# Kernel tuning notes

Hardware: AMD Instinct MI355X
Metric: run time of the kernel (lower is better)

## Reference

```python
import jax, jax.numpy as jnp
import numpy as np

NUM_HEADS = 12
SS_ATTN_ITER = 1
EPS = 1e-12  # F.normalize default eps


def _l2norm(x):
    n = jnp.linalg.norm(x, axis=-1, keepdims=True)
    return x / jnp.maximum(n, EPS)


def setup_inputs() -> dict:
    key = jax.random.key(0)
    k1, k2, k3, k4 = jax.random.split(key, 4)
    N, B, C = 1569, 8, 768
    x = jax.random.normal(k1, (N, B, C), dtype=jnp.float32)
    Wqkv = jax.random.normal(k2, (3 * C, C), dtype=jnp.float32) * 0.02
    Wproj = jax.random.normal(k3, (C, C), dtype=jnp.float32) * 0.02
    bproj = jax.random.normal(k4, (C,), dtype=jnp.float32) * 0.02
    return {"x": x, "Wqkv": Wqkv, "Wproj": Wproj, "bproj": bproj}


def _forward(x, Wqkv, Wproj, bproj):
    # x: [N, B, C] -> [B, N, C] (module does x.transpose(0, 1))
    xb = jnp.swapaxes(x, 0, 1)
    B, N, C = xb.shape
    H = NUM_HEADS
    hd = C // H
    scale = hd ** (-0.5)

    # qkv projection (no bias), split into per-head q, k, v: [B, H, N, hd]
    qkv = (xb @ Wqkv.T).reshape(B, N, 3, H, hd)
    qkv = jnp.transpose(qkv, (2, 0, 3, 1, 4))
    q, k, v = qkv[0], qkv[1], qkv[2]

    # ---- original attention branch ----
    attn_ori = jax.nn.softmax(jnp.einsum('bhnd,bhmd->bhnm', q, k) * scale, axis=-1)
    x_ori = jnp.einsum('bhnm,bhmd->bhnd', attn_ori, v)
    x_ori = jnp.transpose(x_ori, (0, 2, 1, 3)).reshape(B, N, C)
    x_ori = x_ori @ Wproj.T + bproj

    # ---- self-self attention branches ----
    # inv_temp = mean over tokens of ||x||_2, per batch: [B, 1, 1, 1]
    pre_norm = jnp.mean(jnp.linalg.norm(xb, axis=-1), axis=-1)
    inv_temp = pre_norm[:, None, None, None] * scale

    def branch(xs):
        for _ in range(SS_ATTN_ITER):
            xs = _l2norm(xs)
            a = jax.nn.softmax(jnp.einsum('bhnd,bhmd->bhnm', xs, xs) * inv_temp, axis=-1)
            xs = jnp.einsum('bhnm,bhmd->bhnd', a, xs)
        xs = _l2norm(xs)
        a = jax.nn.softmax(jnp.einsum('bhnd,bhmd->bhnm', xs, xs) * inv_temp, axis=-1)
        return jnp.einsum('bhnm,bhmd->bhnd', a, v)

    xs = (branch(v) + branch(k) + branch(q)) / 3.0
    x_out = jnp.transpose(xs, (0, 2, 1, 3)).reshape(B, N, C)
    x_out = x_out @ Wproj.T + bproj

    # return in original [N, B, C] layout
    return jnp.swapaxes(x_out, 0, 1), jnp.swapaxes(x_ori, 0, 1)


def reference(x, Wqkv, Wproj, bproj):
    return _forward(x, Wqkv, Wproj, bproj)
```

## Files before the change

kernel.cpp:

```cpp
#include <hip/hip_runtime.h>
#include <stdint.h>

#define NTOK 1569
#define BB 8
#define CC 768
#define HH 12
#define HD 64
#define NBH (BB*HH)
#define NROW (NTOK*BB)
#define NCHUNK 25
#define NVEC (NBH*NTOK)
#define LASTV 33

typedef unsigned short ushort_t;
static const size_t SZ = (size_t)NROW * CC;

using f32x4 = __attribute__((ext_vector_type(4))) float;
using i32x4 = __attribute__((ext_vector_type(4))) int;
using i32x2 = __attribute__((ext_vector_type(2))) int;
using hfrag = __attribute__((ext_vector_type(8))) _Float16;

__device__ __forceinline__ float exp2_fast(float x){
  float r;
  asm("v_exp_f32 %0, %1" : "=v"(r) : "v"(x));
  return r;
}

__global__ __launch_bounds__(256) void prenorm_kernel(const float* __restrict__ x,
                                                      float* __restrict__ pre)
{
  const int b = blockIdx.y;
  const int wave = threadIdx.x >> 6, lane = threadIdx.x & 63;
  const int g = blockIdx.x * 4 + wave;
  float local = 0.f;
  for (int n = g; n < NTOK; n += 200){
    const float* xp = x + ((size_t)n * BB + b) * CC + lane * 4;
    float ss = 0.f;
    #pragma unroll
    for (int e = 0; e < 3; e++){
      f32x4 vv = *(const f32x4*)(xp + 256*e);
      ss += vv[0]*vv[0] + vv[1]*vv[1] + vv[2]*vv[2] + vv[3]*vv[3];
    }
    #pragma unroll
    for (int off = 1; off < 64; off <<= 1) ss += __shfl_xor(ss, off);
    local += sqrtf(ss);
  }
  if (lane == 0) atomicAdd(&pre[b], local);
}

__global__ __launch_bounds__(256) void cvt_f16(const float* __restrict__ in,
                                               ushort_t* __restrict__ out,
                                               int n8, float scl)
{
  const int i = blockIdx.x * 256 + threadIdx.x;
  if (i >= n8) return;
  const float* p = in + (size_t)i * 8;
  f32x4 a = *(const f32x4*)p, b = *(const f32x4*)(p + 4);
  union { _Float16 h[8]; i32x4 v; } u;
  #pragma unroll
  for (int e = 0; e < 4; e++){
    u.h[e]   = (_Float16)(a[e] * scl);
    u.h[4+e] = (_Float16)(b[e] * scl);
  }
  *(i32x4*)(out + (size_t)i * 8) = u.v;
}

__global__ __launch_bounds__(256) void gemm768(
    const ushort_t* __restrict__ A, const ushort_t* __restrict__ Bm,
    ushort_t* __restrict__ q, ushort_t* __restrict__ k, ushort_t* __restrict__ v,
    float* __restrict__ outp, const float* __restrict__ bias, int mode)
{
  __shared__ __align__(16) ushort_t As[8192];
  __shared__ __align__(16) ushort_t Bs[8192];

  const int mt = blockIdx.x, jt = blockIdx.y;
  const int tid = threadIdx.x;
  const int w = tid >> 6, lane = tid & 63;
  const int l16 = lane & 15, lq = lane >> 4;

  const int srow = tid & 127, shalf = tid >> 7;
  int ga = mt*128 + srow; if (ga > NROW-1) ga = NROW-1;
  const ushort_t* ap = A  + (size_t)ga * CC + shalf*32;
  const ushort_t* bp = Bm + (size_t)(jt*128 + srow) * CC + shalf*32;
  const int rb = srow >> 4, r16 = srow & 15;

  const int wr = (w >> 1) * 4, wc = (w & 1) * 4;

  f32x4 acc[4][4] = {};
  for (int kt = 0; kt < 12; kt++){
    #pragma unroll
    for (int i = 0; i < 4; i++){
      const int kq = shalf*4 + i;
      *(i32x4*)&As[((rb*8 + kq)*16 + r16)*8] = *(const i32x4*)(ap + kt*64 + i*8);
      *(i32x4*)&Bs[((rb*8 + kq)*16 + r16)*8] = *(const i32x4*)(bp + kt*64 + i*8);
    }
    __syncthreads();
    #pragma unroll
    for (int ks = 0; ks < 2; ks++){
      hfrag af[4], bf[4];
      #pragma unroll
      for (int rt = 0; rt < 4; rt++)
        af[rt] = *(const hfrag*)&As[(((wr+rt)*8 + ks*4 + lq)*16 + l16)*8];
      #pragma unroll
      for (int ct = 0; ct < 4; ct++)
        bf[ct] = *(const hfrag*)&Bs[(((wc+ct)*8 + ks*4 + lq)*16 + l16)*8];
      #pragma unroll
      for (int rt = 0; rt < 4; rt++)
        #pragma unroll
        for (int ct = 0; ct < 4; ct++)
          acc[rt][ct] = __builtin_amdgcn_mfma_f32_16x16x32_f16(af[rt], bf[ct], acc[rt][ct], 0, 0, 0);
    }
    __syncthreads();
  }

  const int mbase = mt*128 + (w >> 1)*64;
  const int jbase = jt*128 + (w & 1)*64;
  #pragma unroll
  for (int ct = 0; ct < 4; ct++){
    const int j = jbase + ct*16 + l16;
    if (mode == 0){
      const int s = j / 768, jj = j - s*768;
      const int h = jj >> 6, d = jj & 63;
      ushort_t* op = (s == 0) ? q : (s == 1) ? k : v;
      #pragma unroll
      for (int rt = 0; rt < 4; rt++)
        #pragma unroll
        for (int r = 0; r < 4; r++){
          const int m = mbase + rt*16 + lq*4 + r;
          if (m < NROW){
            const int n = m >> 3, b = m & 7;
            union { _Float16 h16; ushort_t u; } cv;
            cv.h16 = (_Float16)acc[rt][ct][r];
            op[((size_t)(b*HH + h) * NTOK + n) * HD + d] = cv.u;
          }
        }
    } else {
      const float bv = bias[j];
      #pragma unroll
      for (int rt = 0; rt < 4; rt++)
        #pragma unroll
        for (int r = 0; r < 4; r++){
          const int m = mbase + rt*16 + lq*4 + r;
          if (m < NROW) outp[(size_t)m * CC + j] = acc[rt][ct][r] + bv;
        }
    }
  }
}

__global__ __launch_bounds__(256) void l2norm_kernel(const ushort_t* __restrict__ in,
                                                     ushort_t* __restrict__ out,
                                                     int mode)
{
  const int vec = blockIdx.x * 8 + (threadIdx.x >> 5);
  const int lane = threadIdx.x & 31;
  if (vec >= NVEC) return;
  size_t iaddr;
  if (mode == 0){
    iaddr = (size_t)vec * HD + lane*2;
  } else {
    const int b = vec / (HH*NTOK);
    const int rem = vec - b*(HH*NTOK);
    const int h = rem / NTOK, n = rem - h*NTOK;
    iaddr = (size_t)(n*BB + b) * CC + h*HD + lane*2;
  }
  union { ushort_t u[2]; uint32_t pk; _Float16 h[2]; } uv;
  uv.pk = *(const uint32_t*)(in + iaddr);
  const float a = (float)uv.h[0], c = (float)uv.h[1];
  float ss = a*a + c*c;
  #pragma unroll
  for (int off = 1; off < 32; off <<= 1) ss += __shfl_xor(ss, off);
  const float inv = 1.0f / fmaxf(sqrtf(ss), 1e-12f);
  union { _Float16 h[2]; uint32_t pk; } ov;
  ov.h[0] = (_Float16)(a * inv);
  ov.h[1] = (_Float16)(c * inv);
  *(uint32_t*)(out + (size_t)vec * HD + lane*2) = ov.pk;
}

__global__ __launch_bounds__(256) void attn_mfma(
    const ushort_t* __restrict__ X, const ushort_t* __restrict__ Y,
    const ushort_t* __restrict__ Z, void* __restrict__ outp,
    const float* __restrict__ pre, float tf, int mode, int accum)
{
  __shared__ __align__(16) ushort_t Ks[64*64];
  __shared__ __align__(16) ushort_t Vt[64*64];
  __shared__ __align__(16) ushort_t Pt[128*64];

  const int lin  = blockIdx.y * 13 + blockIdx.x;
  const int nl   = (lin & 7) * 156 + (lin >> 3);
  const int bh   = nl / 13;
  const int qblk = nl - bh * 13;

  const int b = bh / HH, h = bh - (bh / HH) * HH;
  const float temp = (pre ? pre[b] * tf : tf) * 1.4426950408889634f;
  const size_t base = (size_t)bh * NTOK * HD;
  const int row0 = qblk * 128;
  const int tid = threadIdx.x;
  const int w = tid >> 6, lane = tid & 63;
  const int l16 = lane & 15, lq = lane >> 4;
  const int xk = (l16 & 7) << 4;

  hfrag qf[2][2];
  #pragma unroll
  for (int qt = 0; qt < 2; qt++){
    int r = row0 + w*32 + qt*16 + l16; if (r > NTOK-1) r = NTOK-1;
    const ushort_t* qp = X + base + (size_t)r*HD + lq*8;
    qf[qt][0] = *(const hfrag*)qp;
    qf[qt][1] = *(const hfrag*)(qp + 32);
  }

  const int skey = tid & 63, sseg = tid >> 6;
  const int kx = (skey & 7) << 4;
  const int vd2 = (tid & 31) * 2;
  const int vko = (tid >> 5) * 8;

  f32x4 acc[2][4] = {};
  float lsum[2] = {0.f, 0.f};

  for (int ch = 0; ch < NCHUNK; ch++){
    {
      int kg = ch*64 + skey; if (kg > NTOK-1) kg = NTOK-1;
      const ushort_t* kp = Y + base + (size_t)kg*HD + sseg*16;
      i32x4 kr0 = *(const i32x4*)kp;
      i32x4 kr1 = *(const i32x4*)(kp + 8);
      char* kbp = (char*)Ks + skey*128;
      *(i32x4*)(kbp + ((sseg*32     ) ^ kx)) = kr0;
      *(i32x4*)(kbp + ((sseg*32 + 16) ^ kx)) = kr1;

      uint32_t L[8];
      #pragma unroll
      for (int j = 0; j < 8; j++){
        int vg = ch*64 + vko + j; if (vg > NTOK-1) vg = NTOK-1;
        L[j] = *(const uint32_t*)(Z + base + (size_t)vg*HD + vd2);
      }
      i32x4 vlo, vhi;
      #pragma unroll
      for (int c = 0; c < 4; c++){
        const uint32_t A = L[2*c], B = L[2*c+1];
        vlo[c] = (int)((A & 0xffffu) | (B << 16));
        vhi[c] = (int)((A >> 16) | (B & 0xffff0000u));
      }
      char* vbp = (char*)Vt;
      *(i32x4*)(vbp + vd2*128     + ((vko*2) ^ ((vd2 & 7) << 4)))       = vlo;
      *(i32x4*)(vbp + (vd2+1)*128 + ((vko*2) ^ (((vd2+1) & 7) << 4)))   = vhi;
    }
    __syncthreads();

    const bool lastch = (ch == NCHUNK-1);
    #pragma unroll
    for (int kt4 = 0; kt4 < 4; kt4++){
      f32x4 s0 = {}, s1 = {};
      #pragma unroll
      for (int ks = 0; ks < 2; ks++){
        hfrag kf = *(const hfrag*)((const char*)Ks + (kt4*16 + l16)*128
                                   + ((ks*64 + lq*16) ^ xk));
        s0 = __builtin_amdgcn_mfma_f32_16x16x32_f16(kf, qf[0][ks], s0, 0, 0, 0);
        s1 = __builtin_amdgcn_mfma_f32_16x16x32_f16(kf, qf[1][ks], s1, 0, 0, 0);
      }
      const int kb = kt4*16 + lq*4;
      #pragma unroll
      for (int qt = 0; qt < 2; qt++){
        const f32x4 sv = qt ? s1 : s0;
        float p0 = exp2_fast(sv[0] * temp);
        float p1 = exp2_fast(sv[1] * temp);
        float p2 = exp2_fast(sv[2] * temp);
        float p3 = exp2_fast(sv[3] * temp);
        if (lastch){
          if (kb + 0 >= LASTV) p0 = 0.f;
          if (kb + 1 >= LASTV) p1 = 0.f;
          if (kb + 2 >= LASTV) p2 = 0.f;
          if (kb + 3 >= LASTV) p3 = 0.f;
        }
        lsum[qt] += p0 + p1 + p2 + p3;
        union { _Float16 hh[4]; i32x2 v2; } pw;
        pw.hh[0] = (_Float16)p0; pw.hh[1] = (_Float16)p1;
        pw.hh[2] = (_Float16)p2; pw.hh[3] = (_Float16)p3;
        *(i32x2*)((char*)Pt + (w*32 + qt*16 + l16)*128
                  + ((kt4*32 + lq*8) ^ xk)) = pw.v2;
      }
    }

    #pragma unroll
    for (int ks = 0; ks < 2; ks++){
      const int cb = (ks*64 + lq*16) ^ xk;
      hfrag pa0 = *(const hfrag*)((const char*)Pt + (w*32 +      l16)*128 + cb);
      hfrag pa1 = *(const hfrag*)((const char*)Pt + (w*32 + 16 + l16)*128 + cb);
      #pragma unroll
      for (int dt4 = 0; dt4 < 4; dt4++){
        hfrag vf = *(const hfrag*)((const char*)Vt + (dt4*16 + l16)*128 + cb);
        acc[0][dt4] = __builtin_amdgcn_mfma_f32_16x16x32_f16(pa0, vf, acc[0][dt4], 0, 0, 0);
        acc[1][dt4] = __builtin_amdgcn_mfma_f32_16x16x32_f16(pa1, vf, acc[1][dt4], 0, 0, 0);
      }
    }
    __syncthreads();
  }

  float lfin[2];
  #pragma unroll
  for (int qt = 0; qt < 2; qt++){
    float lt = lsum[qt];
    lt += __shfl_xor(lt, 16);
    lt += __shfl_xor(lt, 32);
    lfin[qt] = lt;
  }

  #pragma unroll
  for (int qt = 0; qt < 2; qt++)
    #pragma unroll
    for (int r = 0; r < 4; r++){
      const float lv = __int_as_float(
          __builtin_amdgcn_ds_bpermute((lq*4 + r) * 4, __float_as_int(lfin[qt])));
      const int n = row0 + w*32 + qt*16 + lq*4 + r;
      if (n < NTOK){
        const float inv = 1.0f / lv;
        const size_t rbase = (size_t)(n*BB + b) * CC + h*HD;
        if (mode == 0){
          ushort_t* yo = (ushort_t*)outp;
          #pragma unroll
          for (int dt4 = 0; dt4 < 4; dt4++){
            union { _Float16 h16; ushort_t u; } cv;
            cv.h16 = (_Float16)(acc[qt][dt4][r] * inv);
            yo[rbase + dt4*16 + l16] = cv.u;
          }
        } else {
          float* ao = (float*)outp;
          #pragma unroll
          for (int dt4 = 0; dt4 < 4; dt4++){
            float o = acc[qt][dt4][r] * inv;
            if (accum) o += ao[rbase + dt4*16 + l16];
            ao[rbase + dt4*16 + l16] = o;
          }
        }
      }
    }
}

extern "C" void kernel_launch(void* const* d_in, const int* in_sizes, int n_in,
                              void* d_out, int out_size, void* d_ws, size_t ws_size,
                              hipStream_t stream)
{
  (void)in_sizes; (void)n_in; (void)out_size; (void)ws_size;

  const float* x     = (const float*)d_in[0];
  const float* wqkv  = (const float*)d_in[1];
  const float* wproj = (const float*)d_in[2];
  const float* bias  = (const float*)d_in[3];
  float* out = (float*)d_out;

  ushort_t* x16  = (ushort_t*)d_ws;
  ushort_t* wq16 = x16 + SZ;
  ushort_t* wp16 = wq16 + (size_t)2304*768;
  ushort_t* qb   = wp16 + (size_t)768*768;
  ushort_t* kb   = qb + SZ;
  ushort_t* vb   = kb + SZ;
  ushort_t* xh   = vb + SZ;
  ushort_t* y16  = xh + SZ;
  float*    acc  = (float*)(y16 + SZ);
  float*    pre  = acc + SZ;

  hipMemsetAsync(pre, 0, BB * sizeof(float), stream);

  cvt_f16<<<(int)(SZ/8 + 255)/256, 256, 0, stream>>>(x, x16, (int)(SZ/8), 1.0f);
  cvt_f16<<<(2304*768/8 + 255)/256, 256, 0, stream>>>(wqkv, wq16, 2304*768/8, 1.0f);
  cvt_f16<<<(768*768/8 + 255)/256, 256, 0, stream>>>(wproj, wp16, 768*768/8, 1.0f);
  prenorm_kernel<<<dim3(50, 8), 256, 0, stream>>>(x, pre);

  gemm768<<<dim3(99, 18), 256, 0, stream>>>(x16, wq16, qb, kb, vb, nullptr, nullptr, 0);

  const float SCALE = 0.125f;
  const float FACT  = SCALE / (float)NTOK;
  const dim3 AG(13, 96);

  attn_mfma<<<AG, 256, 0, stream>>>(qb, kb, vb, y16, nullptr, SCALE, 0, 0);
  gemm768<<<dim3(99, 6), 256, 0, stream>>>(y16, wp16, nullptr, nullptr, nullptr,
      out + (size_t)NTOK * BB * CC, bias, 1);

  const ushort_t* srcs[3] = { qb, kb, vb };
  for (int sI = 0; sI < 3; sI++){
    l2norm_kernel<<<NVEC/8, 256, 0, stream>>>(srcs[sI], xh, 0);
    attn_mfma<<<AG, 256, 0, stream>>>(xh, xh, xh, y16, pre, FACT, 0, 0);
    l2norm_kernel<<<NVEC/8, 256, 0, stream>>>(y16, xh, 1);
    attn_mfma<<<AG, 256, 0, stream>>>(xh, xh, vb, acc, pre, FACT, 1, sI == 0 ? 0 : 1);
  }

  cvt_f16<<<(int)(SZ/8 + 255)/256, 256, 0, stream>>>(acc, y16, (int)(SZ/8), 1.0f/3.0f);
  gemm768<<<dim3(99, 6), 256, 0, stream>>>(y16, wp16, nullptr, nullptr, nullptr,
      out, bias, 1);
}
```

Baseline: 1.247 ms.

## Prefetch next K/V chunk into registers and remap GEMM blocks for XCD locality

The attention kernel now issues global loads for the next K/V chunk into registers before computing the current chunk, then writes them to shared memory after the compute barrier. This hides global load latency behind the MFMA and softmax work, at the cost of extra registers and an added barrier per iteration. Separately, the GEMM kernel remaps its linear block index so that consecutive tiles land on the same XCD (blocks are chunked in groups of eight), aiming to improve L2 reuse of A and B tiles. The remap hardcodes 99 M-tiles in the grid.

```diff
diff --git a/kernel.cpp b/kernel.cpp
--- a/kernel.cpp
+++ b/kernel.cpp
@@ -73,7 +73,15 @@
   __shared__ __align__(16) ushort_t As[8192];
   __shared__ __align__(16) ushort_t Bs[8192];
 
-  const int mt = blockIdx.x, jt = blockIdx.y;
+  const int jtN = gridDim.y;
+  const int lin = blockIdx.y * 99 + blockIdx.x;
+  const int T  = 99 * jtN;
+  const int qq = T >> 3, rr = T & 7;
+  const int c  = lin & 7, ii = lin >> 3;
+  const int start = c*qq + (c < rr ? c : rr);
+  const int idx = start + ii;
+  const int mt = idx / jtN, jt = idx - mt*jtN;
+
   const int tid = threadIdx.x;
   const int w = tid >> 6, lane = tid & 63;
   const int l16 = lane & 15, lq = lane >> 4;
@@ -213,37 +221,45 @@
   const int vd2 = (tid & 31) * 2;
   const int vko = (tid >> 5) * 8;
 
+  i32x4 kr0, kr1;
+  uint32_t L[8];
+
+  auto LOADR = [&](int ch){
+    int kg = ch*64 + skey; if (kg > NTOK-1) kg = NTOK-1;
+    const ushort_t* kp = Y + base + (size_t)kg*HD + sseg*16;
+    kr0 = *(const i32x4*)kp;
+    kr1 = *(const i32x4*)(kp + 8);
+    #pragma unroll
+    for (int j = 0; j < 8; j++){
+      int vg = ch*64 + vko + j; if (vg > NTOK-1) vg = NTOK-1;
+      L[j] = *(const uint32_t*)(Z + base + (size_t)vg*HD + vd2);
+    }
+  };
+  auto STORER = [&](){
+    char* kbp = (char*)Ks + skey*128;
+    *(i32x4*)(kbp + ((sseg*32     ) ^ kx)) = kr0;
+    *(i32x4*)(kbp + ((sseg*32 + 16) ^ kx)) = kr1;
+    i32x4 vlo, vhi;
+    #pragma unroll
+    for (int cc = 0; cc < 4; cc++){
+      const uint32_t Aw = L[2*cc], Bw = L[2*cc+1];
+      vlo[cc] = (int)((Aw & 0xffffu) | (Bw << 16));
+      vhi[cc] = (int)((Aw >> 16) | (Bw & 0xffff0000u));
+    }
+    char* vbp = (char*)Vt;
+    *(i32x4*)(vbp + vd2*128     + ((vko*2) ^ ((vd2 & 7) << 4)))     = vlo;
+    *(i32x4*)(vbp + (vd2+1)*128 + ((vko*2) ^ (((vd2+1) & 7) << 4))) = vhi;
+  };
+
   f32x4 acc[2][4] = {};
   float lsum[2] = {0.f, 0.f};
 
+  LOADR(0);
+  STORER();
+  __syncthreads();
+
   for (int ch = 0; ch < NCHUNK; ch++){
-    {
-      int kg = ch*64 + skey; if (kg > NTOK-1) kg = NTOK-1;
-      const ushort_t* kp = Y + base + (size_t)kg*HD + sseg*16;
-      i32x4 kr0 = *(const i32x4*)kp;
-      i32x4 kr1 = *(const i32x4*)(kp + 8);
-      char* kbp = (char*)Ks + skey*128;
-      *(i32x4*)(kbp + ((sseg*32     ) ^ kx)) = kr0;
-      *(i32x4*)(kbp + ((sseg*32 + 16) ^ kx)) = kr1;
-
-      uint32_t L[8];
-      #pragma unroll
-      for (int j = 0; j < 8; j++){
-        int vg = ch*64 + vko + j; if (vg > NTOK-1) vg = NTOK-1;
-        L[j] = *(const uint32_t*)(Z + base + (size_t)vg*HD + vd2);
-      }
-      i32x4 vlo, vhi;
-      #pragma unroll
-      for (int c = 0; c < 4; c++){
-        const uint32_t A = L[2*c], B = L[2*c+1];
-        vlo[c] = (int)((A & 0xffffu) | (B << 16));
-        vhi[c] = (int)((A >> 16) | (B & 0xffff0000u));
-      }
-      char* vbp = (char*)Vt;
-      *(i32x4*)(vbp + vd2*128     + ((vko*2) ^ ((vd2 & 7) << 4)))       = vlo;
-      *(i32x4*)(vbp + (vd2+1)*128 + ((vko*2) ^ (((vd2+1) & 7) << 4)))   = vhi;
-    }
-    __syncthreads();
+    if (ch + 1 < NCHUNK) LOADR(ch + 1);
 
     const bool lastch = (ch == NCHUNK-1);
     #pragma unroll
@@ -292,6 +308,10 @@
       }
     }
     __syncthreads();
+    if (ch + 1 < NCHUNK){
+      STORER();
+      __syncthreads();
+    }
   }
 
   float lfin[2];
```

Result: faster. 1.192 ms (-4.4%).
